# Kernel optimization log

Measured on AMD Instinct MI355X. Metric: run time of the kernel, lower is better.

Reference implementation:

```python
import jax, jax.numpy as jnp
import numpy as np

IMAGE_SIZE = (128, 128)
NUM_SLICES = 4
SLICE_SPACING = 0.1
BACKGROUND = 0.0
CHUNK = 1024
N_GAUSS = 4096
EPS = 1e-6


def setup_inputs() -> dict:
    key = jax.random.key(0)
    k1, k2, k3, k4, k5 = jax.random.split(key, 5)
    return {
        "means": jax.random.uniform(k1, (N_GAUSS, 3), dtype=jnp.float32),
        "scales": jax.random.uniform(k2, (N_GAUSS, 3), dtype=jnp.float32),
        "rotations": jax.random.normal(k3, (N_GAUSS, 4), dtype=jnp.float32),
        "opacities": jax.random.uniform(k4, (N_GAUSS, 1), dtype=jnp.float32),
        "features": jax.random.uniform(k5, (N_GAUSS, 1), dtype=jnp.float32),
    }


def _quat_to_rot(q):
    # q: [N,4] (w,x,y,z) -> [N,3,3]
    q = q / jnp.linalg.norm(q, axis=1, keepdims=True)
    w, x, y, z = q[:, 0], q[:, 1], q[:, 2], q[:, 3]
    r0 = jnp.stack([1 - 2 * (y * y + z * z), 2 * (x * y - w * z), 2 * (x * z + w * y)], axis=-1)
    r1 = jnp.stack([2 * (x * y + w * z), 1 - 2 * (x * x + z * z), 2 * (y * z - w * x)], axis=-1)
    r2 = jnp.stack([2 * (x * z - w * y), 2 * (y * z + w * x), 1 - 2 * (x * x + y * y)], axis=-1)
    return jnp.stack([r0, r1, r2], axis=-2)


def _forward(means, scales, rotations, opacities, features):
    H, W = IMAGE_SIZE
    dtype = means.dtype
    P = H * W

    # 3D covariance: Sigma = (R S)(R S)^T
    R = _quat_to_rot(rotations)
    RS = R * scales[:, None, :]
    cov = RS @ jnp.swapaxes(RS, 1, 2)  # [N,3,3]

    # slice z positions and shared pixel grid
    total_depth = (NUM_SLICES - 1) * SLICE_SPACING
    zs = jnp.linspace(-total_depth / 2, total_depth / 2, NUM_SLICES)
    yy, xx = jnp.meshgrid(jnp.linspace(-1, 1, H), jnp.linspace(-1, 1, W), indexing="ij")
    grid = jnp.stack([xx, yy], axis=-1).reshape(P, 2).astype(dtype)

    # conditional (marginal-at-z) 2D covariance, slice independent
    sxy = cov[:, :2, :2]                     # [N,2,2]
    sxz = cov[:, :2, 2]                      # [N,2]
    szz = cov[:, 2, 2]                       # [N]
    sigma2d = sxy - (sxz[:, :, None] * sxz[:, None, :]) / (szz + EPS)[:, None, None]
    sigma2d = sigma2d + EPS * jnp.eye(2, dtype=dtype)
    a, b = sigma2d[:, 0, 0], sigma2d[:, 0, 1]
    c, d = sigma2d[:, 1, 0], sigma2d[:, 1, 1]
    det = a * d - b * c
    inv2d = jnp.stack([jnp.stack([d, -b], -1), jnp.stack([-c, a], -1)], -2) / det[:, None, None]

    max_dist = 3.0 * scales[:, 2].max()

    nch = N_GAUSS // CHUNK
    rs = lambda t: t.reshape((nch, CHUNK) + t.shape[1:])
    chunks = (rs(means), rs(inv2d), rs(sxz), rs(szz), rs(opacities[:, 0]), rs(features[:, 0]))

    def render_slice(slice_z):
        def body(carry, ch):
            img, acc = carry
            mu, invk, sxzk, szzk, op, ft = ch
            mask = (jnp.abs(mu[:, 2] - slice_z) < max_dist).astype(dtype)  # all-pass by construction
            zoff = slice_z - mu[:, 2]
            mu2d = mu[:, :2] + sxzk / (szzk + EPS)[:, None] * zoff[:, None]  # [K,2]
            off = grid[:, None, :] - mu2d[None, :, :]                        # [P,K,2]
            maha = jnp.einsum("pki,kij,pkj->pk", off, invk, off)
            g = jnp.exp(-0.5 * maha) * mask[None, :]                         # [P,K]
            weight = (1 - acc)[:, None] * (g * op[None, :])
            img = img + (weight * (g * ft[None, :])).sum(-1)
            acc = acc + weight.sum(-1)
            return (img, acc), None

        init = (jnp.zeros(P, dtype), jnp.zeros(P, dtype))
        (img, acc), _ = jax.lax.scan(body, init, chunks)
        img = img + (1 - acc) * BACKGROUND
        return img.reshape(H, W)

    return jnp.stack([render_slice(zs[s]) for s in range(NUM_SLICES)], axis=0)


def reference(means, scales, rotations, opacities, features):
    return _forward(means, scales, rotations, opacities, features)
```

## Files before the change

### kernel.cpp

```cpp
#include <hip/hip_runtime.h>


#define EPSV 1e-6f
#define NG   4096
#define PP   16384
#define NSL  4
#define SEGS 8
#define GSEG 128

typedef float v2f __attribute__((ext_vector_type(2)));

static __device__ __forceinline__ v2f splat(float s) { v2f r; r.x = s; r.y = s; return r; }

__global__ void prep_kernel(const float* __restrict__ means,
                            const float* __restrict__ scales,
                            const float* __restrict__ rots,
                            const float* __restrict__ ops,
                            const float* __restrict__ fts,
                            float4* __restrict__ gdata) {
    __shared__ float red[256];
    int tid = threadIdx.x;

    float m = -1e30f;
    for (int i = tid; i < NG; i += 256) m = fmaxf(m, scales[i*3+2]);
    red[tid] = m;
    __syncthreads();
    for (int s = 128; s > 0; s >>= 1) {
        if (tid < s) red[tid] = fmaxf(red[tid], red[tid+s]);
        __syncthreads();
    }
    float maxd = 3.0f * red[0];

    int g = blockIdx.x * 256 + tid;
    if (g >= NG) return;

    float qw = rots[g*4+0], qx = rots[g*4+1], qy = rots[g*4+2], qz = rots[g*4+3];
    float inorm = rsqrtf(qw*qw + qx*qx + qy*qy + qz*qz);
    qw *= inorm; qx *= inorm; qy *= inorm; qz *= inorm;

    float s0 = scales[g*3+0], s1 = scales[g*3+1], s2 = scales[g*3+2];

    float r00 = 1.f - 2.f*(qy*qy + qz*qz), r01 = 2.f*(qx*qy - qw*qz), r02 = 2.f*(qx*qz + qw*qy);
    float r10 = 2.f*(qx*qy + qw*qz), r11 = 1.f - 2.f*(qx*qx + qz*qz), r12 = 2.f*(qy*qz - qw*qx);
    float r20 = 2.f*(qx*qz - qw*qy), r21 = 2.f*(qy*qz + qw*qx), r22 = 1.f - 2.f*(qx*qx + qy*qy);

    float a00 = r00*s0, a01 = r01*s1, a02 = r02*s2;
    float a10 = r10*s0, a11 = r11*s1, a12 = r12*s2;
    float a20 = r20*s0, a21 = r21*s1, a22 = r22*s2;

    float c00 = a00*a00 + a01*a01 + a02*a02;
    float c01 = a00*a10 + a01*a11 + a02*a12;
    float c02 = a00*a20 + a01*a21 + a02*a22;
    float c11 = a10*a10 + a11*a11 + a12*a12;
    float c12 = a10*a20 + a11*a21 + a12*a22;
    float c22 = a20*a20 + a21*a21 + a22*a22;

    float izz = 1.0f / (c22 + EPSV);
    float kx = c02 * izz, ky = c12 * izz;
    float sa = c00 - c02*c02*izz + EPSV;
    float sb = c01 - c02*c12*izz;
    float sd = c11 - c12*c12*izz + EPSV;
    float det = sa*sd - sb*sb;
    float idet = 1.0f / det;

    const float C0 = -0.72134752044448170f;
    float qa = C0 * sd * idet;
    float qb = C0 * (-2.0f * sb * idet);
    float qd = C0 * sa * idet;

    float mx = means[g*3+0], my = means[g*3+1], mz = means[g*3+2];
    float op = ops[g], ft = fts[g];

    #pragma unroll
    for (int s = 0; s < NSL; ++s) {
        float z = -0.15f + 0.1f * (float)s;
        float zoff = z - mz;
        float m2x = mx + kx * zoff;
        float m2y = my + ky * zoff;
        bool live = (fabsf(mz - z) < maxd) && (op > 1e-12f);
        float lop  = live ? __log2f(op) : -__builtin_inff();
        float ftop = live ? ft / op     : 0.f;
        float4* o = gdata + ((size_t)(s*NG + g)) * 2;
        o[0] = make_float4(-m2x, -m2y, qa, qb);
        o[1] = make_float4( qd,   lop,  ftop, 0.f);
    }
}

__global__ __launch_bounds__(1024, 8)
void render_kernel(const float4* __restrict__ gdata, float2* __restrict__ part) {
    int tid   = threadIdx.x;
    int lane  = tid & 63;
    int w     = __builtin_amdgcn_readfirstlane(tid >> 6);
    int b     = blockIdx.x;
    int pxg   = b >> 5;
    int split = b & 31;
    int slice = pxg >> 2;
    int r0    = (pxg & 3) * 32 + w * 2;
    int chunk = split >> 3;
    int seg   = split & 7;

    const float DL = 2.0f / 127.0f;
    v2f xP;  xP.x = -1.0f + (float)lane * DL;  xP.y = xP.x + 64.0f * DL;
    v2f yP0 = splat(-1.0f + (float)r0 * DL);
    v2f yP1 = splat(-1.0f + (float)(r0 + 1) * DL);

    const float4* p = gdata + ((size_t)slice * NG + chunk * 1024 + seg * GSEG) * 2;

    v2f a10 = {0.f,0.f}, a11 = {0.f,0.f}, a20 = {0.f,0.f}, a21 = {0.f,0.f};
    #pragma unroll 8
    for (int g = 0; g < GSEG; ++g) {
        float4 A = p[2*g+0];
        float4 B = p[2*g+1];
        v2f dx  = xP  + splat(A.x);
        v2f dy0 = yP0 + splat(A.y);
        v2f dy1 = yP1 + splat(A.y);
        v2f t0  = __builtin_elementwise_fma(splat(A.z), dx, splat(A.w) * dy0);
        v2f t1  = __builtin_elementwise_fma(splat(A.z), dx, splat(A.w) * dy1);
        v2f e0  = __builtin_elementwise_fma(splat(B.x) * dy0, dy0, splat(B.y));
        v2f e1  = __builtin_elementwise_fma(splat(B.x) * dy1, dy1, splat(B.y));
        v2f mm0 = __builtin_elementwise_fma(dx, t0, e0);
        v2f mm1 = __builtin_elementwise_fma(dx, t1, e1);
        v2f gv0, gv1;
        gv0.x = __builtin_amdgcn_exp2f(mm0.x);
        gv0.y = __builtin_amdgcn_exp2f(mm0.y);
        gv1.x = __builtin_amdgcn_exp2f(mm1.x);
        gv1.y = __builtin_amdgcn_exp2f(mm1.y);
        a10 += gv0;
        a11 += gv1;
        a20 = __builtin_elementwise_fma(gv0 * gv0, splat(B.z), a20);
        a21 = __builtin_elementwise_fma(gv1 * gv1, splat(B.z), a21);
    }

    size_t o = ((size_t)(slice * PP + r0 * 128 + lane)) * 32 + chunk * 8 + seg;
    part[o           ] = make_float2(a10.x, a20.x);
    part[o +  64 * 32] = make_float2(a10.y, a20.y);
    part[o + 128 * 32] = make_float2(a11.x, a21.x);
    part[o + 192 * 32] = make_float2(a11.y, a21.y);
}

__global__ __launch_bounds__(256)
void combine_kernel(const float2* __restrict__ part, float* __restrict__ out) {
    int px = blockIdx.x * 256 + threadIdx.x;
    const float2* q = part + (size_t)px * 32;
    float img = 0.f, acc = 0.f;
    #pragma unroll
    for (int c = 0; c < 4; ++c) {
        float S1 = 0.f, S2 = 0.f;
        #pragma unroll
        for (int s = 0; s < SEGS; ++s) {
            float2 v = q[c*8 + s];
            S1 += v.x;  S2 += v.y;
        }
        float om = 1.0f - acc;
        img = fmaf(om, S2, img);
        acc = fmaf(om, S1, acc);
    }
    out[px] = img;
}

extern "C" void kernel_launch(void* const* d_in, const int* in_sizes, int n_in,
                              void* d_out, int out_size, void* d_ws, size_t ws_size,
                              hipStream_t stream) {
    const float* means  = (const float*)d_in[0];
    const float* scales = (const float*)d_in[1];
    const float* rots   = (const float*)d_in[2];
    const float* ops    = (const float*)d_in[3];
    const float* fts    = (const float*)d_in[4];
    float* out = (float*)d_out;

    float4* gdata = (float4*)d_ws;
    float2* part  = (float2*)((char*)d_ws + (size_t)NSL*NG*32);

    prep_kernel<<<NG/256, 256, 0, stream>>>(means, scales, rots, ops, fts, gdata);
    render_kernel<<<512, 1024, 0, stream>>>(gdata, part);
    combine_kernel<<<NSL*PP/256, 256, 0, stream>>>(part, out);
}
```

Baseline: 128.7 us.

## Expand quadratic form into polynomial coefficients and restructure render tiling

Prep now precomputes the Gaussian exponent as a polynomial in x and y (quadratic, linear and constant coefficients with log-opacity folded in). This lets the render inner loop drop the per-pixel offset subtractions and use nested FMAs. Render blocks shrink to 512 threads over 16-row bands, and each wave walks the 128-Gaussian segment in 16-Gaussian sub-blocks starting at a wave-staggered offset, likely to spread load traffic. Partial sums move to a chunk-major layout so the combine kernel reads coalesced. The expanded polynomial can lose floating-point precision through cancellation.

```diff
diff --git a/kernel.cpp b/kernel.cpp
--- a/kernel.cpp
+++ b/kernel.cpp
@@ -5,12 +5,8 @@
 #define NG   4096
 #define PP   16384
 #define NSL  4
-#define SEGS 8
 #define GSEG 128
-
-typedef float v2f __attribute__((ext_vector_type(2)));
-
-static __device__ __forceinline__ v2f splat(float s) { v2f r; r.x = s; r.y = s; return r; }
+#define SUBB 16
 
 __global__ void prep_kernel(const float* __restrict__ means,
                             const float* __restrict__ scales,
@@ -80,75 +76,81 @@
         bool live = (fabsf(mz - z) < maxd) && (op > 1e-12f);
         float lop  = live ? __log2f(op) : -__builtin_inff();
         float ftop = live ? ft / op     : 0.f;
+        float c3 = -(2.0f*qa*m2x + qb*m2y);
+        float c4 = -(2.0f*qd*m2y + qb*m2x);
+        float c5 = qa*m2x*m2x + qb*m2x*m2y + qd*m2y*m2y + lop;
         float4* o = gdata + ((size_t)(s*NG + g)) * 2;
-        o[0] = make_float4(-m2x, -m2y, qa, qb);
-        o[1] = make_float4( qd,   lop,  ftop, 0.f);
+        o[0] = make_float4(qa, qb, qd, c3);
+        o[1] = make_float4(c4, c5, ftop, 0.f);
     }
 }
 
-__global__ __launch_bounds__(1024, 8)
+__global__ __launch_bounds__(512, 8)
 void render_kernel(const float4* __restrict__ gdata, float2* __restrict__ part) {
     int tid   = threadIdx.x;
     int lane  = tid & 63;
     int w     = __builtin_amdgcn_readfirstlane(tid >> 6);
     int b     = blockIdx.x;
-    int pxg   = b >> 5;
-    int split = b & 31;
-    int slice = pxg >> 2;
-    int r0    = (pxg & 3) * 32 + w * 2;
-    int chunk = split >> 3;
-    int seg   = split & 7;
+    int cs    = b & 31;
+    int band  = b >> 5;
+    int slice = band >> 3;
+    int r0    = (band & 7) * 16 + w * 2;
 
     const float DL = 2.0f / 127.0f;
-    v2f xP;  xP.x = -1.0f + (float)lane * DL;  xP.y = xP.x + 64.0f * DL;
-    v2f yP0 = splat(-1.0f + (float)r0 * DL);
-    v2f yP1 = splat(-1.0f + (float)(r0 + 1) * DL);
+    float x0 = -1.0f + (float)lane * DL;
+    float x1 = x0 + 64.0f * DL;
+    float y0 = -1.0f + (float)r0 * DL;
+    float y1 = y0 + DL;
 
-    const float4* p = gdata + ((size_t)slice * NG + chunk * 1024 + seg * GSEG) * 2;
+    const float4* base = gdata + ((size_t)slice * NG + cs * GSEG) * 2;
 
-    v2f a10 = {0.f,0.f}, a11 = {0.f,0.f}, a20 = {0.f,0.f}, a21 = {0.f,0.f};
-    #pragma unroll 8
-    for (int g = 0; g < GSEG; ++g) {
-        float4 A = p[2*g+0];
-        float4 B = p[2*g+1];
-        v2f dx  = xP  + splat(A.x);
-        v2f dy0 = yP0 + splat(A.y);
-        v2f dy1 = yP1 + splat(A.y);
-        v2f t0  = __builtin_elementwise_fma(splat(A.z), dx, splat(A.w) * dy0);
-        v2f t1  = __builtin_elementwise_fma(splat(A.z), dx, splat(A.w) * dy1);
-        v2f e0  = __builtin_elementwise_fma(splat(B.x) * dy0, dy0, splat(B.y));
-        v2f e1  = __builtin_elementwise_fma(splat(B.x) * dy1, dy1, splat(B.y));
-        v2f mm0 = __builtin_elementwise_fma(dx, t0, e0);
-        v2f mm1 = __builtin_elementwise_fma(dx, t1, e1);
-        v2f gv0, gv1;
-        gv0.x = __builtin_amdgcn_exp2f(mm0.x);
-        gv0.y = __builtin_amdgcn_exp2f(mm0.y);
-        gv1.x = __builtin_amdgcn_exp2f(mm1.x);
-        gv1.y = __builtin_amdgcn_exp2f(mm1.y);
-        a10 += gv0;
-        a11 += gv1;
-        a20 = __builtin_elementwise_fma(gv0 * gv0, splat(B.z), a20);
-        a21 = __builtin_elementwise_fma(gv1 * gv1, splat(B.z), a21);
+    float a100 = 0.f, a101 = 0.f, a110 = 0.f, a111 = 0.f;
+    float a200 = 0.f, a201 = 0.f, a210 = 0.f, a211 = 0.f;
+
+    for (int kk = 0; kk < 8; ++kk) {
+        int sb = (w + kk) & 7;
+        const float4* q = base + sb * SUBB * 2;
+        #pragma unroll 8
+        for (int j = 0; j < SUBB; ++j) {
+            float4 A = q[2*j+0];
+            float4 B = q[2*j+1];
+            float T0 = fmaf(A.y, y0, A.w);
+            float T1 = fmaf(A.y, y1, A.w);
+            float R0 = fmaf(fmaf(A.z, y0, B.x), y0, B.y);
+            float R1 = fmaf(fmaf(A.z, y1, B.x), y1, B.y);
+            float m00 = fmaf(fmaf(A.x, x0, T0), x0, R0);
+            float m01 = fmaf(fmaf(A.x, x1, T0), x1, R0);
+            float m10 = fmaf(fmaf(A.x, x0, T1), x0, R1);
+            float m11 = fmaf(fmaf(A.x, x1, T1), x1, R1);
+            float g00 = __builtin_amdgcn_exp2f(m00);
+            float g01 = __builtin_amdgcn_exp2f(m01);
+            float g10 = __builtin_amdgcn_exp2f(m10);
+            float g11 = __builtin_amdgcn_exp2f(m11);
+            a100 += g00;  a101 += g01;  a110 += g10;  a111 += g11;
+            a200 = fmaf(g00*g00, B.z, a200);
+            a201 = fmaf(g01*g01, B.z, a201);
+            a210 = fmaf(g10*g10, B.z, a210);
+            a211 = fmaf(g11*g11, B.z, a211);
+        }
     }
 
-    size_t o = ((size_t)(slice * PP + r0 * 128 + lane)) * 32 + chunk * 8 + seg;
-    part[o           ] = make_float2(a10.x, a20.x);
-    part[o +  64 * 32] = make_float2(a10.y, a20.y);
-    part[o + 128 * 32] = make_float2(a11.x, a21.x);
-    part[o + 192 * 32] = make_float2(a11.y, a21.y);
+    size_t o = (size_t)cs * (NSL * PP) + slice * PP + r0 * 128 + lane;
+    part[o      ] = make_float2(a100, a200);
+    part[o +  64] = make_float2(a101, a201);
+    part[o + 128] = make_float2(a110, a210);
+    part[o + 192] = make_float2(a111, a211);
 }
 
 __global__ __launch_bounds__(256)
 void combine_kernel(const float2* __restrict__ part, float* __restrict__ out) {
     int px = blockIdx.x * 256 + threadIdx.x;
-    const float2* q = part + (size_t)px * 32;
     float img = 0.f, acc = 0.f;
     #pragma unroll
     for (int c = 0; c < 4; ++c) {
         float S1 = 0.f, S2 = 0.f;
         #pragma unroll
-        for (int s = 0; s < SEGS; ++s) {
-            float2 v = q[c*8 + s];
+        for (int s = 0; s < 8; ++s) {
+            float2 v = part[(size_t)(c*8 + s) * (NSL*PP) + px];
             S1 += v.x;  S2 += v.y;
         }
         float om = 1.0f - acc;
@@ -172,6 +174,6 @@
     float2* part  = (float2*)((char*)d_ws + (size_t)NSL*NG*32);
 
     prep_kernel<<<NG/256, 256, 0, stream>>>(means, scales, rots, ops, fts, gdata);
-    render_kernel<<<512, 1024, 0, stream>>>(gdata, part);
+    render_kernel<<<1024, 512, 0, stream>>>(gdata, part);
     combine_kernel<<<NSL*PP/256, 256, 0, stream>>>(part, out);
 }
```

Result: no change. 128.9 us (+0.2%).
